# Kernel optimization log

Measured on AMD Instinct MI355X. Metric: run time of the kernel, lower is better.

The kernel has to match this reference:

```python
import jax, jax.numpy as jnp
import numpy as np

D_MODEL = 1024
HEADS = 16
D_K = D_MODEL // HEADS


def setup_inputs() -> dict:
    key = jax.random.key(0)
    ks = jax.random.split(key, 11)
    bs, seq = 2, 2048
    scale = 1.0 / np.sqrt(D_MODEL)
    inp = {
        "query": jax.random.normal(ks[0], (bs, seq, D_MODEL), jnp.float32),
        "key": jax.random.normal(ks[1], (bs, seq, D_MODEL), jnp.float32),
        "value": jax.random.normal(ks[2], (bs, seq, D_MODEL), jnp.float32),
        # nn.Linear weights: y = x @ W.T + b, W shape [out, in]
        "Wq": jax.random.normal(ks[3], (D_MODEL, D_MODEL), jnp.float32) * scale,
        "bq": jnp.zeros((D_MODEL,), jnp.float32),
        "Wk": jax.random.normal(ks[4], (D_MODEL, D_MODEL), jnp.float32) * scale,
        "bk": jnp.zeros((D_MODEL,), jnp.float32),
        "Wv": jax.random.normal(ks[5], (D_MODEL, D_MODEL), jnp.float32) * scale,
        "bv": jnp.zeros((D_MODEL,), jnp.float32),
        "Wo": jax.random.normal(ks[6], (D_MODEL, D_MODEL), jnp.float32) * scale,
        "bo": jnp.zeros((D_MODEL,), jnp.float32),
    }
    return inp


def _split_heads(x, bs):
    # [b, s, d_model] -> [b, h, s, d_k]
    return x.reshape(bs, -1, HEADS, D_K).transpose(0, 2, 1, 3)


def reference(query, key, value, Wq, bq, Wk, bk, Wv, bv, Wo, bo):
    bs = query.shape[0]
    q = _split_heads(query @ Wq.T + bq, bs)
    k = _split_heads(key @ Wk.T + bk, bs)
    v = _split_heads(value @ Wv.T + bv, bs)
    # scaled dot-product attention (dropout is identity at eval)
    logits = jnp.einsum("bhqd,bhkd->bhqk", q, k) / np.sqrt(D_K).astype(np.float32)
    probs = jax.nn.softmax(logits, axis=-1)
    scores = jnp.einsum("bhqk,bhkd->bhqd", probs, v)  # [b, h, s, d_k]
    concat = scores.transpose(0, 2, 1, 3).reshape(bs, -1, D_MODEL)
    output = concat @ Wo.T + bo
    return (output, scores)
```

## Files before the change

kernel.cpp:

```cpp
#include <hip/hip_runtime.h>
#include <stdint.h>
#include <math.h>

typedef __bf16 bf16;
typedef __bf16 bf16x4 __attribute__((ext_vector_type(4)));
typedef __bf16 bf16x8 __attribute__((ext_vector_type(8)));
typedef float floatx4 __attribute__((ext_vector_type(4)));

#define CEXP 0.1803368801111204f

__global__ __launch_bounds__(256) void wcvt_kernel(
    const float* __restrict__ Wq, const float* __restrict__ Wk,
    const float* __restrict__ Wv, const float* __restrict__ Wo,
    bf16* __restrict__ dst)
{
  const float* src = (blockIdx.y == 0) ? Wq : (blockIdx.y == 1) ? Wk
                   : (blockIdx.y == 2) ? Wv : Wo;
  bf16* d = dst + (size_t)blockIdx.y * 1048576;
  const int i = (blockIdx.x * 256 + threadIdx.x) * 4;
  const floatx4 v = *(const floatx4*)(src + i);
  bf16x4 o;
#pragma unroll
  for (int j = 0; j < 4; ++j) o[j] = (bf16)v[j];
  *(bf16x4*)(d + i) = o;
}

__device__ __forceinline__ void gemm_body(
    const float* __restrict__ A, const bf16* __restrict__ Ab,
    const bf16* __restrict__ Wb, const float* __restrict__ bias,
    void* __restrict__ Cout, const int mode, const float oscale)
{
  __shared__ __align__(16) bf16 As[128 * 72];
  __shared__ __align__(16) bf16 Bs[128 * 72];
  const int tid  = threadIdx.x;
  const int wave = tid >> 6;
  const int lane = tid & 63;
  const int mlane = lane & 15;
  const int quad  = lane >> 4;
  const int m0 = blockIdx.x * 128;
  const int n0 = blockIdx.y * 128;
  const int wm = (wave >> 1) * 64;
  const int wn = (wave & 1) * 64;
  const int arow = tid >> 4, ac4 = (tid & 15) * 4;
  const int wrow = tid >> 3, wc8 = (tid & 7) * 8;

  floatx4 a_pf[8];
  bf16x8  ab_pf[4];
  bf16x8  w_pf[4];

  auto load_a = [&](int k0) {
    if (mode == 1) {
#pragma unroll
      for (int c = 0; c < 4; ++c) {
        const int token = m0 + c * 32 + wrow;
        const int b = token >> 11, s = token & 2047;
        const int h = k0 >> 6;
        ab_pf[c] = *(const bf16x8*)(Ab + (((size_t)(b * 16 + h) * 2048 + s) << 6) + wc8);
      }
    } else {
#pragma unroll
      for (int rr = 0; rr < 8; ++rr)
        a_pf[rr] = *(const floatx4*)(A + (size_t)(m0 + rr * 16 + arow) * 1024 + k0 + ac4);
    }
  };
  auto load_w = [&](int k0) {
#pragma unroll
    for (int c = 0; c < 4; ++c)
      w_pf[c] = *(const bf16x8*)(Wb + (size_t)(n0 + c * 32 + wrow) * 1024 + k0 + wc8);
  };

  load_a(0);
  load_w(0);

  floatx4 acc[4][4] = {};

  for (int k0 = 0; k0 < 1024; k0 += 64) {
    if (mode == 1) {
#pragma unroll
      for (int c = 0; c < 4; ++c)
        *(bf16x8*)&As[(c * 32 + wrow) * 72 + wc8] = ab_pf[c];
    } else {
#pragma unroll
      for (int rr = 0; rr < 8; ++rr) {
        bf16x4 ac;
#pragma unroll
        for (int j = 0; j < 4; ++j) ac[j] = (bf16)a_pf[rr][j];
        *(bf16x4*)&As[(rr * 16 + arow) * 72 + ac4] = ac;
      }
    }
#pragma unroll
    for (int c = 0; c < 4; ++c)
      *(bf16x8*)&Bs[(c * 32 + wrow) * 72 + wc8] = w_pf[c];
    __syncthreads();

    if (k0 + 64 < 1024) { load_a(k0 + 64); load_w(k0 + 64); }

#pragma unroll
    for (int kk = 0; kk < 64; kk += 32) {
      bf16x8 af[4], bfr[4];
#pragma unroll
      for (int t = 0; t < 4; ++t) {
        af[t]  = *(const bf16x8*)&As[(wm + t * 16 + mlane) * 72 + kk + quad * 8];
        bfr[t] = *(const bf16x8*)&Bs[(wn + t * 16 + mlane) * 72 + kk + quad * 8];
      }
#pragma unroll
      for (int mt = 0; mt < 4; ++mt)
#pragma unroll
        for (int nt = 0; nt < 4; ++nt)
          acc[mt][nt] = __builtin_amdgcn_mfma_f32_16x16x32_bf16(
              af[mt], bfr[nt], acc[mt][nt], 0, 0, 0);
    }
    __syncthreads();
  }

#pragma unroll
  for (int nt = 0; nt < 4; ++nt) {
    const int col = n0 + wn + nt * 16 + mlane;
    const float bv = bias[col];
#pragma unroll
    for (int mt = 0; mt < 4; ++mt) {
#pragma unroll
      for (int r = 0; r < 4; ++r) {
        const int row = m0 + wm + mt * 16 + quad * 4 + r;
        const float v = (acc[mt][nt][r] + bv) * oscale;
        if (mode == 0) {
          const int b = row >> 11, s = row & 2047;
          const int h = col >> 6, dk = col & 63;
          ((bf16*)Cout)[(((size_t)(b * 16 + h) * 2048 + s) << 6) + dk] = (bf16)v;
        } else if (mode == 2) {
          const int b = row >> 11, s = row & 2047;
          const int h = col >> 6, dk = col & 63;
          ((bf16*)Cout)[(((size_t)(b * 16 + h) * 64 + dk) << 11) + s] = (bf16)v;
        } else {
          ((float*)Cout)[(size_t)row * 1024 + col] = v;
        }
      }
    }
  }
}

__global__ __launch_bounds__(256) void qkv_kernel(
    const float* __restrict__ q, const float* __restrict__ k, const float* __restrict__ v,
    const bf16* __restrict__ Wb,
    const float* __restrict__ bq, const float* __restrict__ bk, const float* __restrict__ bv,
    bf16* __restrict__ Qw, bf16* __restrict__ Kw, bf16* __restrict__ Vw)
{
  const int z = blockIdx.z;
  const float* A = (z == 0) ? q : (z == 1) ? k : v;
  const bf16* W  = Wb + (size_t)z * 1048576;
  const float* B = (z == 0) ? bq : (z == 1) ? bk : bv;
  if (z == 2)      gemm_body(A, nullptr, W, B, Vw, 2, 1.0f);
  else if (z == 1) gemm_body(A, nullptr, W, B, Kw, 0, 1.0f);
  else             gemm_body(A, nullptr, W, B, Qw, 0, CEXP);
}

__global__ __launch_bounds__(256) void out_kernel(
    const bf16* __restrict__ Sb, const bf16* __restrict__ Wob,
    const float* __restrict__ bo, float* __restrict__ out)
{
  gemm_body(nullptr, Sb, Wob, bo, out, 1, 1.0f);
}

__global__ __launch_bounds__(256) void attn_kernel(
    const bf16* __restrict__ Qw, const bf16* __restrict__ Kw,
    const bf16* __restrict__ Vtg, float* __restrict__ scores,
    bf16* __restrict__ Sb)
{
  __shared__ __align__(16) bf16 Ks[64 * 72];
  __shared__ __align__(16) bf16 Vt[64 * 72];
  __shared__ __align__(16) bf16 Ps[4][32 * 72];

  const int tid  = threadIdx.x;
  const int wave = tid >> 6;
  const int lane = tid & 63;
  const int mlane = lane & 15;
  const int quad  = lane >> 4;
  const int bh = blockIdx.y;
  const int q0 = blockIdx.x * 128;
  const size_t base = (size_t)bh << 17;

  const int srow = tid >> 3, sc8 = (tid & 7) * 8;

  bf16x8 qf[2][2];
#pragma unroll
  for (int qt = 0; qt < 2; ++qt)
#pragma unroll
    for (int c = 0; c < 2; ++c)
      qf[qt][c] = *(const bf16x8*)
          &Qw[base + (size_t)(q0 + wave * 32 + qt * 16 + mlane) * 64 + c * 32 + quad * 8];

  float rs[2] = {0.f, 0.f};
  floatx4 o[2][4] = {};

  bf16x8 kpf[2], vpf[2];
  auto load_kv = [&](int kt) {
#pragma unroll
    for (int rr = 0; rr < 2; ++rr) {
      const int row = rr * 32 + srow;
      kpf[rr] = *(const bf16x8*)&Kw[base + (size_t)(kt + row) * 64 + sc8];
      vpf[rr] = *(const bf16x8*)&Vtg[base + (size_t)row * 2048 + kt + sc8];
    }
  };
  load_kv(0);

  for (int kt = 0; kt < 2048; kt += 64) {
    __syncthreads();
#pragma unroll
    for (int rr = 0; rr < 2; ++rr) {
      const int row = rr * 32 + srow;
      *(bf16x8*)&Ks[row * 72 + sc8] = kpf[rr];
      *(bf16x8*)&Vt[row * 72 + sc8] = vpf[rr];
    }
    __syncthreads();
    if (kt + 64 < 2048) load_kv(kt + 64);

#pragma unroll
    for (int nt = 0; nt < 4; ++nt) {
      bf16x8 a0 = *(const bf16x8*)&Ks[(nt * 16 + mlane) * 72 + quad * 8];
      bf16x8 a1 = *(const bf16x8*)&Ks[(nt * 16 + mlane) * 72 + 32 + quad * 8];
      floatx4 s0 = {}, s1 = {};
      s0 = __builtin_amdgcn_mfma_f32_16x16x32_bf16(a0, qf[0][0], s0, 0, 0, 0);
      s0 = __builtin_amdgcn_mfma_f32_16x16x32_bf16(a1, qf[0][1], s0, 0, 0, 0);
      s1 = __builtin_amdgcn_mfma_f32_16x16x32_bf16(a0, qf[1][0], s1, 0, 0, 0);
      s1 = __builtin_amdgcn_mfma_f32_16x16x32_bf16(a1, qf[1][1], s1, 0, 0, 0);

      bf16x4 pk0, pk1;
#pragma unroll
      for (int r = 0; r < 4; ++r) {
        const float p0 = exp2f(s0[r]);
        const float p1 = exp2f(s1[r]);
        rs[0] += p0; rs[1] += p1;
        pk0[r] = (bf16)p0; pk1[r] = (bf16)p1;
      }
      *(bf16x4*)&Ps[wave][(mlane)      * 72 + nt * 16 + quad * 4] = pk0;
      *(bf16x4*)&Ps[wave][(16 + mlane) * 72 + nt * 16 + quad * 4] = pk1;
    }

    asm volatile("s_waitcnt lgkmcnt(0)" ::: "memory");

#pragma unroll
    for (int c = 0; c < 2; ++c) {
      bf16x8 pa0 = *(const bf16x8*)&Ps[wave][(mlane)      * 72 + c * 32 + quad * 8];
      bf16x8 pa1 = *(const bf16x8*)&Ps[wave][(16 + mlane) * 72 + c * 32 + quad * 8];
#pragma unroll
      for (int nt = 0; nt < 4; ++nt) {
        bf16x8 vb = *(const bf16x8*)&Vt[(nt * 16 + mlane) * 72 + c * 32 + quad * 8];
        o[0][nt] = __builtin_amdgcn_mfma_f32_16x16x32_bf16(pa0, vb, o[0][nt], 0, 0, 0);
        o[1][nt] = __builtin_amdgcn_mfma_f32_16x16x32_bf16(pa1, vb, o[1][nt], 0, 0, 0);
      }
    }
  }

#pragma unroll
  for (int qt = 0; qt < 2; ++qt) {
    rs[qt] += __shfl_xor(rs[qt], 16, 64);
    rs[qt] += __shfl_xor(rs[qt], 32, 64);
  }
  const float inv0 = 1.0f / rs[0];
  const float inv1 = 1.0f / rs[1];

#pragma unroll
  for (int qt = 0; qt < 2; ++qt) {
#pragma unroll
    for (int r = 0; r < 4; ++r) {
      const float invr = __shfl(qt ? inv1 : inv0, quad * 4 + r, 64);
      const int row = q0 + wave * 32 + qt * 16 + quad * 4 + r;
#pragma unroll
      for (int nt = 0; nt < 4; ++nt) {
        const float val = o[qt][nt][r] * invr;
        const size_t idx = base + (size_t)row * 64 + nt * 16 + mlane;
        scores[idx] = val;
        Sb[idx] = (bf16)val;
      }
    }
  }
}

extern "C" void kernel_launch(void* const* d_in, const int* in_sizes, int n_in,
                              void* d_out, int out_size, void* d_ws, size_t ws_size,
                              hipStream_t stream) {
  const float* query = (const float*)d_in[0];
  const float* key   = (const float*)d_in[1];
  const float* value = (const float*)d_in[2];
  const float* Wq = (const float*)d_in[3];
  const float* bq = (const float*)d_in[4];
  const float* Wk = (const float*)d_in[5];
  const float* bk = (const float*)d_in[6];
  const float* Wv = (const float*)d_in[7];
  const float* bv = (const float*)d_in[8];
  const float* Wo = (const float*)d_in[9];
  const float* bo = (const float*)d_in[10];

  float* out    = (float*)d_out;
  float* scores = out + (size_t)4194304;

  bf16* Wb  = (bf16*)d_ws;
  bf16* Qws = Wb + (size_t)4194304;
  bf16* Kws = Qws + (size_t)4194304;
  bf16* Vws = Kws + (size_t)4194304;
  bf16* Sb  = Vws + (size_t)4194304;

  wcvt_kernel<<<dim3(1024, 4), 256, 0, stream>>>(Wq, Wk, Wv, Wo, Wb);
  qkv_kernel<<<dim3(32, 8, 3), 256, 0, stream>>>(query, key, value, Wb,
                                                 bq, bk, bv, Qws, Kws, Vws);
  attn_kernel<<<dim3(16, 32), 256, 0, stream>>>(Qws, Kws, Vws, scores, Sb);
  out_kernel<<<dim3(32, 8), 256, 0, stream>>>(Sb, Wb + (size_t)3145728, bo, out);
}
```

Before: 247.8 us.

## Halve GEMM M-tile and load attention K fragments directly into registers

The projection GEMMs move from 128x128 to 64x128 block tiles and double their grid in M, giving more blocks for the CUs on the QKV and output projections. In the attention kernel the K tile no longer goes through shared memory. Each wave loads its MFMA K fragments straight from global memory into double-buffered registers, removing LDS stores and reads for K. The trade-offs are more register pressure and redundant K loads across the four waves, plus less reuse of W per block in the GEMMs.

```diff
diff --git a/kernel.cpp b/kernel.cpp
--- a/kernel.cpp
+++ b/kernel.cpp
@@ -30,28 +30,28 @@
     const bf16* __restrict__ Wb, const float* __restrict__ bias,
     void* __restrict__ Cout, const int mode, const float oscale)
 {
-  __shared__ __align__(16) bf16 As[128 * 72];
+  __shared__ __align__(16) bf16 As[64 * 72];
   __shared__ __align__(16) bf16 Bs[128 * 72];
   const int tid  = threadIdx.x;
   const int wave = tid >> 6;
   const int lane = tid & 63;
   const int mlane = lane & 15;
   const int quad  = lane >> 4;
-  const int m0 = blockIdx.x * 128;
+  const int m0 = blockIdx.x * 64;
   const int n0 = blockIdx.y * 128;
-  const int wm = (wave >> 1) * 64;
+  const int wm = (wave >> 1) * 32;
   const int wn = (wave & 1) * 64;
   const int arow = tid >> 4, ac4 = (tid & 15) * 4;
   const int wrow = tid >> 3, wc8 = (tid & 7) * 8;
 
-  floatx4 a_pf[8];
-  bf16x8  ab_pf[4];
+  floatx4 a_pf[4];
+  bf16x8  ab_pf[2];
   bf16x8  w_pf[4];
 
   auto load_a = [&](int k0) {
     if (mode == 1) {
 #pragma unroll
-      for (int c = 0; c < 4; ++c) {
+      for (int c = 0; c < 2; ++c) {
         const int token = m0 + c * 32 + wrow;
         const int b = token >> 11, s = token & 2047;
         const int h = k0 >> 6;
@@ -59,7 +59,7 @@
       }
     } else {
 #pragma unroll
-      for (int rr = 0; rr < 8; ++rr)
+      for (int rr = 0; rr < 4; ++rr)
         a_pf[rr] = *(const floatx4*)(A + (size_t)(m0 + rr * 16 + arow) * 1024 + k0 + ac4);
     }
   };
@@ -72,16 +72,16 @@
   load_a(0);
   load_w(0);
 
-  floatx4 acc[4][4] = {};
+  floatx4 acc[2][4] = {};
 
   for (int k0 = 0; k0 < 1024; k0 += 64) {
     if (mode == 1) {
 #pragma unroll
-      for (int c = 0; c < 4; ++c)
+      for (int c = 0; c < 2; ++c)
         *(bf16x8*)&As[(c * 32 + wrow) * 72 + wc8] = ab_pf[c];
     } else {
 #pragma unroll
-      for (int rr = 0; rr < 8; ++rr) {
+      for (int rr = 0; rr < 4; ++rr) {
         bf16x4 ac;
 #pragma unroll
         for (int j = 0; j < 4; ++j) ac[j] = (bf16)a_pf[rr][j];
@@ -97,14 +97,15 @@
 
 #pragma unroll
     for (int kk = 0; kk < 64; kk += 32) {
-      bf16x8 af[4], bfr[4];
-#pragma unroll
-      for (int t = 0; t < 4; ++t) {
+      bf16x8 af[2], bfr[4];
+#pragma unroll
+      for (int t = 0; t < 2; ++t)
         af[t]  = *(const bf16x8*)&As[(wm + t * 16 + mlane) * 72 + kk + quad * 8];
+#pragma unroll
+      for (int t = 0; t < 4; ++t)
         bfr[t] = *(const bf16x8*)&Bs[(wn + t * 16 + mlane) * 72 + kk + quad * 8];
-      }
-#pragma unroll
-      for (int mt = 0; mt < 4; ++mt)
+#pragma unroll
+      for (int mt = 0; mt < 2; ++mt)
 #pragma unroll
         for (int nt = 0; nt < 4; ++nt)
           acc[mt][nt] = __builtin_amdgcn_mfma_f32_16x16x32_bf16(
@@ -118,7 +119,7 @@
     const int col = n0 + wn + nt * 16 + mlane;
     const float bv = bias[col];
 #pragma unroll
-    for (int mt = 0; mt < 4; ++mt) {
+    for (int mt = 0; mt < 2; ++mt) {
 #pragma unroll
       for (int r = 0; r < 4; ++r) {
         const int row = m0 + wm + mt * 16 + quad * 4 + r;
@@ -166,7 +167,6 @@
     const bf16* __restrict__ Vtg, float* __restrict__ scores,
     bf16* __restrict__ Sb)
 {
-  __shared__ __align__(16) bf16 Ks[64 * 72];
   __shared__ __align__(16) bf16 Vt[64 * 72];
   __shared__ __align__(16) bf16 Ps[4][32 * 72];
 
@@ -192,37 +192,42 @@
   float rs[2] = {0.f, 0.f};
   floatx4 o[2][4] = {};
 
-  bf16x8 kpf[2], vpf[2];
-  auto load_kv = [&](int kt) {
+  bf16x8 vpf[2];
+  bf16x8 kf[2][4][2];
+  auto load_v = [&](int kt) {
 #pragma unroll
     for (int rr = 0; rr < 2; ++rr) {
       const int row = rr * 32 + srow;
-      kpf[rr] = *(const bf16x8*)&Kw[base + (size_t)(kt + row) * 64 + sc8];
       vpf[rr] = *(const bf16x8*)&Vtg[base + (size_t)row * 2048 + kt + sc8];
     }
   };
-  load_kv(0);
-
+  auto load_k = [&](int kt, int buf) {
+#pragma unroll
+    for (int nt = 0; nt < 4; ++nt)
+#pragma unroll
+      for (int c = 0; c < 2; ++c)
+        kf[buf][nt][c] = *(const bf16x8*)
+            &Kw[base + (size_t)(kt + nt * 16 + mlane) * 64 + c * 32 + quad * 8];
+  };
+  load_v(0);
+  load_k(0, 0);
+
+  int cur = 0;
   for (int kt = 0; kt < 2048; kt += 64) {
     __syncthreads();
 #pragma unroll
-    for (int rr = 0; rr < 2; ++rr) {
-      const int row = rr * 32 + srow;
-      *(bf16x8*)&Ks[row * 72 + sc8] = kpf[rr];
-      *(bf16x8*)&Vt[row * 72 + sc8] = vpf[rr];
-    }
+    for (int rr = 0; rr < 2; ++rr)
+      *(bf16x8*)&Vt[(rr * 32 + srow) * 72 + sc8] = vpf[rr];
     __syncthreads();
-    if (kt + 64 < 2048) load_kv(kt + 64);
+    if (kt + 64 < 2048) { load_v(kt + 64); load_k(kt + 64, cur ^ 1); }
 
 #pragma unroll
     for (int nt = 0; nt < 4; ++nt) {
-      bf16x8 a0 = *(const bf16x8*)&Ks[(nt * 16 + mlane) * 72 + quad * 8];
-      bf16x8 a1 = *(const bf16x8*)&Ks[(nt * 16 + mlane) * 72 + 32 + quad * 8];
       floatx4 s0 = {}, s1 = {};
-      s0 = __builtin_amdgcn_mfma_f32_16x16x32_bf16(a0, qf[0][0], s0, 0, 0, 0);
-      s0 = __builtin_amdgcn_mfma_f32_16x16x32_bf16(a1, qf[0][1], s0, 0, 0, 0);
-      s1 = __builtin_amdgcn_mfma_f32_16x16x32_bf16(a0, qf[1][0], s1, 0, 0, 0);
-      s1 = __builtin_amdgcn_mfma_f32_16x16x32_bf16(a1, qf[1][1], s1, 0, 0, 0);
+      s0 = __builtin_amdgcn_mfma_f32_16x16x32_bf16(kf[cur][nt][0], qf[0][0], s0, 0, 0, 0);
+      s0 = __builtin_amdgcn_mfma_f32_16x16x32_bf16(kf[cur][nt][1], qf[0][1], s0, 0, 0, 0);
+      s1 = __builtin_amdgcn_mfma_f32_16x16x32_bf16(kf[cur][nt][0], qf[1][0], s1, 0, 0, 0);
+      s1 = __builtin_amdgcn_mfma_f32_16x16x32_bf16(kf[cur][nt][1], qf[1][1], s1, 0, 0, 0);
 
       bf16x4 pk0, pk1;
 #pragma unroll
@@ -249,6 +254,7 @@
         o[1][nt] = __builtin_amdgcn_mfma_f32_16x16x32_bf16(pa1, vb, o[1][nt], 0, 0, 0);
       }
     }
+    cur ^= 1;
   }
 
 #pragma unroll
@@ -301,8 +307,8 @@
   bf16* Sb  = Vws + (size_t)4194304;
 
   wcvt_kernel<<<dim3(1024, 4), 256, 0, stream>>>(Wq, Wk, Wv, Wo, Wb);
-  qkv_kernel<<<dim3(32, 8, 3), 256, 0, stream>>>(query, key, value, Wb,
+  qkv_kernel<<<dim3(64, 8, 3), 256, 0, stream>>>(query, key, value, Wb,
                                                  bq, bk, bv, Qws, Kws, Vws);
   attn_kernel<<<dim3(16, 32), 256, 0, stream>>>(Qws, Kws, Vws, scores, Sb);
-  out_kernel<<<dim3(32, 8), 256, 0, stream>>>(Sb, Wb + (size_t)3145728, bo, out);
-}
+  out_kernel<<<dim3(64, 8), 256, 0, stream>>>(Sb, Wb + (size_t)3145728, bo, out);
+}
```

After: 369.5 us. 49.1% more time.
